# Performance work log

Hardware: AMD Instinct MI355X
Metric: run time of the kernel (lower is better)

## Reference

```python
import jax, jax.numpy as jnp
import numpy as np

N_NODES = 100000
N_EDGES = 600000
F_IN, HID, CLS = 128, 128, 16


def sage_conv(x, src, dst, W_l, b_l, W_r, n_nodes):
    # mean aggregation of neighbor features: message x[src] scattered to dst
    msg = x[src]                                              # [E, F]
    agg = jax.ops.segment_sum(msg, dst, num_segments=n_nodes)  # [N, F]
    deg = jax.ops.segment_sum(jnp.ones((src.shape[0],), x.dtype), dst, num_segments=n_nodes)
    agg = agg / jnp.maximum(deg, 1.0)[:, None]
    # PyG SAGEConv: lin_l(agg) (with bias) + lin_r(x_root) (no bias)
    return agg @ W_l + b_l + x @ W_r


def setup_inputs() -> dict:
    key = jax.random.key(0)
    ks = jax.random.split(key, 6)
    x = jax.random.normal(ks[0], (N_NODES, F_IN), jnp.float32)
    edge_index = jax.random.randint(ks[1], (2, N_EDGES), 0, N_NODES, dtype=jnp.int64)
    s1 = 1.0 / np.sqrt(F_IN)
    s2 = 1.0 / np.sqrt(HID)
    return {
        "x": x,
        "edge_index": edge_index,
        "W1_l": jax.random.normal(ks[2], (F_IN, HID), jnp.float32) * s1,
        "b1": jnp.zeros((HID,), jnp.float32),
        "W1_r": jax.random.normal(ks[3], (F_IN, HID), jnp.float32) * s1,
        "W2_l": jax.random.normal(ks[4], (HID, CLS), jnp.float32) * s2,
        "b2": jnp.zeros((CLS,), jnp.float32),
        "W2_r": jax.random.normal(ks[5], (HID, CLS), jnp.float32) * s2,
    }


def reference(x, edge_index, W1_l, b1, W1_r, W2_l, b2, W2_r):
    n = x.shape[0]
    src, dst = edge_index[0], edge_index[1]
    h = sage_conv(x, src, dst, W1_l, b1, W1_r, n)
    h = jax.nn.relu(h)
    # F.dropout(training=self.training): identity in eval mode
    out = sage_conv(h, src, dst, W2_l, b2, W2_r, n)
    return jax.nn.log_softmax(out, axis=1)
```

## Files before the change

### kernel.cpp

```cpp
#include <hip/hip_runtime.h>
#include <cstdint>

#define N_NODES 100000
#define N_PAD 100096
#define N_EDGES 600000
#define F 128
#define CLS 16
#define CAP 32

typedef short bf16x8 __attribute__((ext_vector_type(8)));
typedef float f32x4 __attribute__((ext_vector_type(4)));

__device__ inline float bf2f(unsigned int lo16) { return __uint_as_float(lo16 << 16); }
__device__ inline unsigned short f2b(float f) {
    unsigned int u = __float_as_uint(f);
    return (unsigned short)((u + 0x7fffu + ((u >> 16) & 1u)) >> 16);
}

__global__ __launch_bounds__(256) void init_k(int* __restrict__ deg,
                                              const float* __restrict__ x,
                                              unsigned short* __restrict__ xb,
                                              const float* __restrict__ W1l,
                                              const float* __restrict__ W1r,
                                              const float* __restrict__ W2l,
                                              const float* __restrict__ W2r,
                                              unsigned short* __restrict__ w1t,
                                              unsigned short* __restrict__ w2t) {
    int b = blockIdx.x;
    if (b < 98) {
        int i = b * 1024 + threadIdx.x * 4;
#pragma unroll
        for (int k = 0; k < 4; k++)
            if (i + k < N_NODES) deg[i + k] = 0;
    } else if (b < 12598) {
        int i = (b - 98) * 256 + threadIdx.x;
        if (i < N_NODES * F / 4) {
            float4 v = ((const float4*)x)[i];
            ushort4 o;
            o.x = f2b(v.x); o.y = f2b(v.y); o.z = f2b(v.z); o.w = f2b(v.w);
            ((ushort4*)xb)[i] = o;
        }
    } else if (b < 12726) {
        int idx = (b - 12598) * 256 + threadIdx.x;
        int n = idx >> 8, k = idx & 255;
        float v = (k < F) ? W1l[k * F + n] : W1r[(k - F) * F + n];
        int ct = n >> 4, m = n & 15;
        int half = k >> 7, ks = (k >> 5) & 3, quad = (k >> 3) & 3, j = k & 7;
        w1t[(ct * 8 + ks * 2 + half) * 512 + (quad * 16 + m) * 8 + j] = f2b(v);
    } else {
        int idx = (b - 12726) * 256 + threadIdx.x;
        if (idx < 32 * F) {
            int n = idx >> 7, k = idx & 127;
            float v = (n < CLS) ? W2l[k * CLS + n] : W2r[k * CLS + (n - CLS)];
            int tile = n >> 4, m = n & 15;
            int ks = (k >> 5) & 3, quad = (k >> 3) & 3, j = k & 7;
            w2t[(tile * 4 + ks) * 512 + (quad * 16 + m) * 8 + j] = f2b(v);
        }
    }
}

__global__ void fill_k(const int* __restrict__ src, const int* __restrict__ dst,
                       int* __restrict__ deg, int* __restrict__ bucket) {
    int e = blockIdx.x * blockDim.x + threadIdx.x;
    if (e < N_EDGES) {
        int d = dst[e];
        int slot = atomicAdd(&deg[d], 1);
        if (slot < CAP) bucket[d * CAP + slot] = src[e];
    }
}

__global__ __launch_bounds__(256) void gemm_fused(const unsigned short* __restrict__ Xb,
                                                  const int* __restrict__ deg,
                                                  const int* __restrict__ bucket,
                                                  const unsigned short* __restrict__ Wt,
                                                  const float* __restrict__ bias,
                                                  const unsigned short* __restrict__ Wt2,
                                                  unsigned short* __restrict__ trLb,
                                                  float* __restrict__ trR) {
    __shared__ unsigned short sh[128 * 136];
    int tid = threadIdx.x;
    int row0 = blockIdx.x * 128;

    int grp = tid >> 4, l16 = tid & 15, f8 = l16 * 8;
#pragma unroll 1
    for (int rr = 0; rr < 8; rr++) {
        int lr = grp * 8 + rr;
        int node = row0 + lr;
        const int* bk = bucket + (size_t)node * CAP;
        int d_raw = deg[node];
        int4 b0 = *(const int4*)(bk);
        int4 b1 = *(const int4*)(bk + 4);
        int4 b2 = *(const int4*)(bk + 8);
        int d = (node < N_NODES) ? min(max(d_raw, 0), CAP) : 0;
        int n0  = (d > 0)  ? min(max(b0.x, 0), N_NODES - 1) : 0;
        int n1  = (d > 1)  ? min(max(b0.y, 0), N_NODES - 1) : 0;
        int n2  = (d > 2)  ? min(max(b0.z, 0), N_NODES - 1) : 0;
        int n3  = (d > 3)  ? min(max(b0.w, 0), N_NODES - 1) : 0;
        int n4  = (d > 4)  ? min(max(b1.x, 0), N_NODES - 1) : 0;
        int n5  = (d > 5)  ? min(max(b1.y, 0), N_NODES - 1) : 0;
        int n6  = (d > 6)  ? min(max(b1.z, 0), N_NODES - 1) : 0;
        int n7  = (d > 7)  ? min(max(b1.w, 0), N_NODES - 1) : 0;
        int n8  = (d > 8)  ? min(max(b2.x, 0), N_NODES - 1) : 0;
        int n9  = (d > 9)  ? min(max(b2.y, 0), N_NODES - 1) : 0;
        int n10 = (d > 10) ? min(max(b2.z, 0), N_NODES - 1) : 0;
        int n11 = (d > 11) ? min(max(b2.w, 0), N_NODES - 1) : 0;
        uint4 v0  = *(const uint4*)(Xb + (size_t)n0 * F + f8);
        uint4 v1  = *(const uint4*)(Xb + (size_t)n1 * F + f8);
        uint4 v2  = *(const uint4*)(Xb + (size_t)n2 * F + f8);
        uint4 v3  = *(const uint4*)(Xb + (size_t)n3 * F + f8);
        uint4 v4  = *(const uint4*)(Xb + (size_t)n4 * F + f8);
        uint4 v5  = *(const uint4*)(Xb + (size_t)n5 * F + f8);
        uint4 v6  = *(const uint4*)(Xb + (size_t)n6 * F + f8);
        uint4 v7  = *(const uint4*)(Xb + (size_t)n7 * F + f8);
        uint4 v8  = *(const uint4*)(Xb + (size_t)n8 * F + f8);
        uint4 v9  = *(const uint4*)(Xb + (size_t)n9 * F + f8);
        uint4 v10 = *(const uint4*)(Xb + (size_t)n10 * F + f8);
        uint4 v11 = *(const uint4*)(Xb + (size_t)n11 * F + f8);

        float acc[8] = {0.f, 0.f, 0.f, 0.f, 0.f, 0.f, 0.f, 0.f};
#define ACC8(vv) { \
        acc[0] += bf2f((vv).x & 0xffffu); acc[1] += bf2f((vv).x >> 16); \
        acc[2] += bf2f((vv).y & 0xffffu); acc[3] += bf2f((vv).y >> 16); \
        acc[4] += bf2f((vv).z & 0xffffu); acc[5] += bf2f((vv).z >> 16); \
        acc[6] += bf2f((vv).w & 0xffffu); acc[7] += bf2f((vv).w >> 16); }
        if (d > 0)  ACC8(v0);
        if (d > 1)  ACC8(v1);
        if (d > 2)  ACC8(v2);
        if (d > 3)  ACC8(v3);
        if (d > 4)  ACC8(v4);
        if (d > 5)  ACC8(v5);
        if (d > 6)  ACC8(v6);
        if (d > 7)  ACC8(v7);
        if (d > 8)  ACC8(v8);
        if (d > 9)  ACC8(v9);
        if (d > 10) ACC8(v10);
        if (d > 11) ACC8(v11);
        for (int j0 = 12; j0 < d; j0 += 4) {
            int4 bb = *(const int4*)(bk + j0);
            int rem = d - j0;
            int m0 = (rem > 0) ? min(max(bb.x, 0), N_NODES - 1) : 0;
            int m1 = (rem > 1) ? min(max(bb.y, 0), N_NODES - 1) : 0;
            int m2 = (rem > 2) ? min(max(bb.z, 0), N_NODES - 1) : 0;
            int m3 = (rem > 3) ? min(max(bb.w, 0), N_NODES - 1) : 0;
            uint4 w0 = *(const uint4*)(Xb + (size_t)m0 * F + f8);
            uint4 w1 = *(const uint4*)(Xb + (size_t)m1 * F + f8);
            uint4 w2 = *(const uint4*)(Xb + (size_t)m2 * F + f8);
            uint4 w3 = *(const uint4*)(Xb + (size_t)m3 * F + f8);
            if (rem > 0) ACC8(w0);
            if (rem > 1) ACC8(w1);
            if (rem > 2) ACC8(w2);
            if (rem > 3) ACC8(w3);
        }
#undef ACC8
        float inv = 1.0f / fmaxf((float)d, 1.0f);
        uint4 o;
        o.x = (unsigned int)f2b(acc[0] * inv) | ((unsigned int)f2b(acc[1] * inv) << 16);
        o.y = (unsigned int)f2b(acc[2] * inv) | ((unsigned int)f2b(acc[3] * inv) << 16);
        o.z = (unsigned int)f2b(acc[4] * inv) | ((unsigned int)f2b(acc[5] * inv) << 16);
        o.w = (unsigned int)f2b(acc[6] * inv) | ((unsigned int)f2b(acc[7] * inv) << 16);
        *(uint4*)&sh[lr * 136 + f8] = o;
    }
    __syncthreads();

    int wave = tid >> 6, lane = tid & 63;
    int m = lane & 15, quad = lane >> 4;
    int koff = quad * 8;
    int wrow0 = row0 + wave * 32;

    const unsigned short* sa0 = sh + (wave * 32 + m) * 136 + koff;
    const unsigned short* sa1 = sa0 + 16 * 136;
    const unsigned short* px0 = Xb + (size_t)(wrow0 + m) * F + koff;
    const unsigned short* px1 = px0 + 16 * F;
    const unsigned short* pw = Wt + lane * 8;

    f32x4 acc0[8], acc1[8];
#pragma unroll
    for (int ct = 0; ct < 8; ct++) { acc0[ct] = (f32x4){0,0,0,0}; acc1[ct] = (f32x4){0,0,0,0}; }

#pragma unroll
    for (int ks = 0; ks < 4; ks++) {
        bf16x8 a0 = *(const bf16x8*)(const void*)(sa0 + ks * 32);
        bf16x8 a1 = *(const bf16x8*)(const void*)(sa1 + ks * 32);
        bf16x8 x0 = *(const bf16x8*)(const void*)(px0 + ks * 32);
        bf16x8 x1 = *(const bf16x8*)(const void*)(px1 + ks * 32);
#pragma unroll
        for (int ct = 0; ct < 8; ct++) {
            bf16x8 bl = *(const bf16x8*)(const void*)(pw + (ct * 8 + ks * 2 + 0) * 512);
            bf16x8 br = *(const bf16x8*)(const void*)(pw + (ct * 8 + ks * 2 + 1) * 512);
            acc0[ct] = __builtin_amdgcn_mfma_f32_16x16x32_bf16(a0, bl, acc0[ct], 0, 0, 0);
            acc1[ct] = __builtin_amdgcn_mfma_f32_16x16x32_bf16(a1, bl, acc1[ct], 0, 0, 0);
            acc0[ct] = __builtin_amdgcn_mfma_f32_16x16x32_bf16(x0, br, acc0[ct], 0, 0, 0);
            acc1[ct] = __builtin_amdgcn_mfma_f32_16x16x32_bf16(x1, br, acc1[ct], 0, 0, 0);
        }
    }
    __syncthreads();

    int lr0 = wave * 32 + quad * 4;
#pragma unroll
    for (int ct = 0; ct < 8; ct++) {
        int n = ct * 16 + m;
        float bv = bias[n];
#pragma unroll
        for (int r = 0; r < 4; r++) {
            sh[(lr0 + r) * 136 + n]      = f2b(fmaxf(acc0[ct][r] + bv, 0.f));
            sh[(lr0 + 16 + r) * 136 + n] = f2b(fmaxf(acc1[ct][r] + bv, 0.f));
        }
    }
    __syncthreads();

    const unsigned short* hl0 = sh + (wave * 32 + m) * 136 + koff;
    const unsigned short* hl1 = hl0 + 16 * 136;
    const unsigned short* pw2 = Wt2 + lane * 8;

    f32x4 al0 = (f32x4){0,0,0,0}, al1 = (f32x4){0,0,0,0};
    f32x4 ar0 = (f32x4){0,0,0,0}, ar1 = (f32x4){0,0,0,0};
#pragma unroll
    for (int ks = 0; ks < 4; ks++) {
        bf16x8 h0 = *(const bf16x8*)(const void*)(hl0 + ks * 32);
        bf16x8 h1 = *(const bf16x8*)(const void*)(hl1 + ks * 32);
        bf16x8 wl = *(const bf16x8*)(const void*)(pw2 + (0 * 4 + ks) * 512);
        bf16x8 wr = *(const bf16x8*)(const void*)(pw2 + (1 * 4 + ks) * 512);
        al0 = __builtin_amdgcn_mfma_f32_16x16x32_bf16(h0, wl, al0, 0, 0, 0);
        al1 = __builtin_amdgcn_mfma_f32_16x16x32_bf16(h1, wl, al1, 0, 0, 0);
        ar0 = __builtin_amdgcn_mfma_f32_16x16x32_bf16(h0, wr, ar0, 0, 0, 0);
        ar1 = __builtin_amdgcn_mfma_f32_16x16x32_bf16(h1, wr, ar1, 0, 0, 0);
    }
    int r0 = wrow0 + quad * 4;
#pragma unroll
    for (int r = 0; r < 4; r++) {
        trLb[(size_t)(r0 + r) * CLS + m]      = f2b(al0[r]);
        trLb[(size_t)(r0 + 16 + r) * CLS + m] = f2b(al1[r]);
        trR[(size_t)(r0 + r) * CLS + m]       = ar0[r];
        trR[(size_t)(r0 + 16 + r) * CLS + m]  = ar1[r];
    }
}

__global__ __launch_bounds__(256) void agg2sm_k(const unsigned short* __restrict__ trLb,
                                                const float* __restrict__ trR,
                                                const int* __restrict__ deg,
                                                const int* __restrict__ bucket,
                                                const float* __restrict__ b2,
                                                float* __restrict__ out) {
    int node = blockIdx.x * 4 + (threadIdx.x >> 6);
    int lane = threadIdx.x & 63;
    int r = lane >> 2;
    int cq = (lane & 3) * 4;
    const int* bk = bucket + node * CAP;

    int d_raw = deg[node];
    int d = min(d_raw, CAP);
    int nb = (r < d) ? min(max(bk[r], 0), N_NODES - 1) : 0;
    uint2 v = *(const uint2*)(trLb + (size_t)nb * CLS + cq);
    float4 selfR = *(const float4*)(trR + (size_t)node * CLS + cq);

    float4 acc = {0.f, 0.f, 0.f, 0.f};
    if (r < d) {
        acc.x += bf2f(v.x & 0xffffu); acc.y += bf2f(v.x >> 16);
        acc.z += bf2f(v.y & 0xffffu); acc.w += bf2f(v.y >> 16);
    }
    if (d > 16) {
        int idx = 16 + r;
        bool valid = idx < d;
        int m2 = valid ? min(max(bk[idx], 0), N_NODES - 1) : 0;
        uint2 w = *(const uint2*)(trLb + (size_t)m2 * CLS + cq);
        if (valid) {
            acc.x += bf2f(w.x & 0xffffu); acc.y += bf2f(w.x >> 16);
            acc.z += bf2f(w.y & 0xffffu); acc.w += bf2f(w.y >> 16);
        }
    }
#pragma unroll
    for (int off = 4; off <= 32; off <<= 1) {
        acc.x += __shfl_xor(acc.x, off);
        acc.y += __shfl_xor(acc.y, off);
        acc.z += __shfl_xor(acc.z, off);
        acc.w += __shfl_xor(acc.w, off);
    }
    float inv = 1.0f / fmaxf((float)d, 1.0f);
    float4 bb = *(const float4*)(b2 + cq);
    float vx = acc.x * inv + selfR.x + bb.x;
    float vy = acc.y * inv + selfR.y + bb.y;
    float vz = acc.z * inv + selfR.z + bb.z;
    float vw = acc.w * inv + selfR.w + bb.w;
    float mx = fmaxf(fmaxf(vx, vy), fmaxf(vz, vw));
    mx = fmaxf(mx, __shfl_xor(mx, 1));
    mx = fmaxf(mx, __shfl_xor(mx, 2));
    float sm = __expf(vx - mx) + __expf(vy - mx) + __expf(vz - mx) + __expf(vw - mx);
    sm += __shfl_xor(sm, 1);
    sm += __shfl_xor(sm, 2);
    float lg = __logf(sm);
    if (r == 0) {
        float4 o = {vx - mx - lg, vy - mx - lg, vz - mx - lg, vw - mx - lg};
        *(float4*)(out + (size_t)node * CLS + cq) = o;
    }
}


extern "C" void kernel_launch(void* const* d_in, const int* in_sizes, int n_in,
                              void* d_out, int out_size, void* d_ws, size_t ws_size,
                              hipStream_t stream) {
    const float* x   = (const float*)d_in[0];
    const int*   ei  = (const int*)d_in[1];
    const float* W1l = (const float*)d_in[2];
    const float* b1  = (const float*)d_in[3];
    const float* W1r = (const float*)d_in[4];
    const float* W2l = (const float*)d_in[5];
    const float* b2  = (const float*)d_in[6];
    const float* W2r = (const float*)d_in[7];
    float* out = (float*)d_out;

    const int* src = ei;
    const int* dst = ei + N_EDGES;

    char* ws = (char*)d_ws;
    size_t off = 0;
    auto alloc = [&](size_t bytes) { char* p = ws + off; off += (bytes + 127) / 128 * 128; return p; };
    int* deg    = (int*)alloc((size_t)N_NODES * 4);
    int* bucket = (int*)alloc((size_t)N_NODES * CAP * 4);
    unsigned short* xb   = (unsigned short*)alloc((size_t)N_PAD * F * 2);
    unsigned short* trLb = (unsigned short*)alloc((size_t)N_PAD * CLS * 2);
    float*          trR  = (float*)alloc((size_t)N_PAD * CLS * 4);
    unsigned short* w1t  = (unsigned short*)alloc((size_t)F * 256 * 2);
    unsigned short* w2t  = (unsigned short*)alloc((size_t)32 * F * 2);

    init_k<<<12743, 256, 0, stream>>>(deg, x, xb, W1l, W1r, W2l, W2r, w1t, w2t);
    fill_k<<<(N_EDGES + 255) / 256, 256, 0, stream>>>(src, dst, deg, bucket);
    gemm_fused<<<N_PAD / 128, 256, 0, stream>>>(xb, deg, bucket, w1t, b1, w2t, trLb, trR);
    agg2sm_k<<<N_NODES / 4, 256, 0, stream>>>(trLb, trR, deg, bucket, b2, out);
}
```

Baseline: 217.0 us.

## Stage neighbor buckets in LDS and double-buffer gathers across node rows

Neighbor index lists and degrees for the block's 128 nodes are loaded cooperatively into shared memory up front. The per-row gather loop is then software-pipelined with two register sets, so the 12 feature gathers for the next row are issued before the current row is accumulated. The aim is to hide gather latency and raise memory-level parallelism in the aggregation phase. The cost is many more live VGPRs (two sets of 12 uint4 values), which may reduce occupancy. It also relies on each row's staged bucket being written and read by the same wave, since there is no barrier between staging and use.

```diff
diff --git a/kernel.cpp b/kernel.cpp
--- a/kernel.cpp
+++ b/kernel.cpp
@@ -81,85 +81,127 @@
     int tid = threadIdx.x;
     int row0 = blockIdx.x * 128;
 
+    {
+        int ns = tid >> 1, half = tid & 1;
+        const int4* gsrc = (const int4*)(bucket + (size_t)(row0 + ns) * CAP + half * 16);
+        int* drow = (int*)(sh + ns * 136);
+        int4* ldst = (int4*)(drow + half * 16);
+        ldst[0] = gsrc[0];
+        ldst[1] = gsrc[1];
+        ldst[2] = gsrc[2];
+        ldst[3] = gsrc[3];
+        if (half == 0) drow[32] = deg[row0 + ns];
+    }
+
     int grp = tid >> 4, l16 = tid & 15, f8 = l16 * 8;
-#pragma unroll 1
-    for (int rr = 0; rr < 8; rr++) {
-        int lr = grp * 8 + rr;
-        int node = row0 + lr;
-        const int* bk = bucket + (size_t)node * CAP;
-        int d_raw = deg[node];
-        int4 b0 = *(const int4*)(bk);
-        int4 b1 = *(const int4*)(bk + 4);
-        int4 b2 = *(const int4*)(bk + 8);
-        int d = (node < N_NODES) ? min(max(d_raw, 0), CAP) : 0;
-        int n0  = (d > 0)  ? min(max(b0.x, 0), N_NODES - 1) : 0;
-        int n1  = (d > 1)  ? min(max(b0.y, 0), N_NODES - 1) : 0;
-        int n2  = (d > 2)  ? min(max(b0.z, 0), N_NODES - 1) : 0;
-        int n3  = (d > 3)  ? min(max(b0.w, 0), N_NODES - 1) : 0;
-        int n4  = (d > 4)  ? min(max(b1.x, 0), N_NODES - 1) : 0;
-        int n5  = (d > 5)  ? min(max(b1.y, 0), N_NODES - 1) : 0;
-        int n6  = (d > 6)  ? min(max(b1.z, 0), N_NODES - 1) : 0;
-        int n7  = (d > 7)  ? min(max(b1.w, 0), N_NODES - 1) : 0;
-        int n8  = (d > 8)  ? min(max(b2.x, 0), N_NODES - 1) : 0;
-        int n9  = (d > 9)  ? min(max(b2.y, 0), N_NODES - 1) : 0;
-        int n10 = (d > 10) ? min(max(b2.z, 0), N_NODES - 1) : 0;
-        int n11 = (d > 11) ? min(max(b2.w, 0), N_NODES - 1) : 0;
-        uint4 v0  = *(const uint4*)(Xb + (size_t)n0 * F + f8);
-        uint4 v1  = *(const uint4*)(Xb + (size_t)n1 * F + f8);
-        uint4 v2  = *(const uint4*)(Xb + (size_t)n2 * F + f8);
-        uint4 v3  = *(const uint4*)(Xb + (size_t)n3 * F + f8);
-        uint4 v4  = *(const uint4*)(Xb + (size_t)n4 * F + f8);
-        uint4 v5  = *(const uint4*)(Xb + (size_t)n5 * F + f8);
-        uint4 v6  = *(const uint4*)(Xb + (size_t)n6 * F + f8);
-        uint4 v7  = *(const uint4*)(Xb + (size_t)n7 * F + f8);
-        uint4 v8  = *(const uint4*)(Xb + (size_t)n8 * F + f8);
-        uint4 v9  = *(const uint4*)(Xb + (size_t)n9 * F + f8);
-        uint4 v10 = *(const uint4*)(Xb + (size_t)n10 * F + f8);
-        uint4 v11 = *(const uint4*)(Xb + (size_t)n11 * F + f8);
-
-        float acc[8] = {0.f, 0.f, 0.f, 0.f, 0.f, 0.f, 0.f, 0.f};
+    int lrb = grp * 8;
+
+#define ISSUE(P, DV, LR) do { \
+    const int* brow_ = (const int*)(sh + (LR) * 136); \
+    int node_ = row0 + (LR); \
+    int draw_ = brow_[32]; \
+    DV = (node_ < N_NODES) ? min(max(draw_, 0), CAP) : 0; \
+    int4 b0_ = ((const int4*)brow_)[0]; \
+    int4 b1_ = ((const int4*)brow_)[1]; \
+    int4 b2_ = ((const int4*)brow_)[2]; \
+    int n0_  = (DV > 0 ) ? min(max(b0_.x, 0), N_NODES - 1) : 0; \
+    int n1_  = (DV > 1 ) ? min(max(b0_.y, 0), N_NODES - 1) : 0; \
+    int n2_  = (DV > 2 ) ? min(max(b0_.z, 0), N_NODES - 1) : 0; \
+    int n3_  = (DV > 3 ) ? min(max(b0_.w, 0), N_NODES - 1) : 0; \
+    int n4_  = (DV > 4 ) ? min(max(b1_.x, 0), N_NODES - 1) : 0; \
+    int n5_  = (DV > 5 ) ? min(max(b1_.y, 0), N_NODES - 1) : 0; \
+    int n6_  = (DV > 6 ) ? min(max(b1_.z, 0), N_NODES - 1) : 0; \
+    int n7_  = (DV > 7 ) ? min(max(b1_.w, 0), N_NODES - 1) : 0; \
+    int n8_  = (DV > 8 ) ? min(max(b2_.x, 0), N_NODES - 1) : 0; \
+    int n9_  = (DV > 9 ) ? min(max(b2_.y, 0), N_NODES - 1) : 0; \
+    int n10_ = (DV > 10) ? min(max(b2_.z, 0), N_NODES - 1) : 0; \
+    int n11_ = (DV > 11) ? min(max(b2_.w, 0), N_NODES - 1) : 0; \
+    P##0  = *(const uint4*)(Xb + (size_t)n0_  * F + f8); \
+    P##1  = *(const uint4*)(Xb + (size_t)n1_  * F + f8); \
+    P##2  = *(const uint4*)(Xb + (size_t)n2_  * F + f8); \
+    P##3  = *(const uint4*)(Xb + (size_t)n3_  * F + f8); \
+    P##4  = *(const uint4*)(Xb + (size_t)n4_  * F + f8); \
+    P##5  = *(const uint4*)(Xb + (size_t)n5_  * F + f8); \
+    P##6  = *(const uint4*)(Xb + (size_t)n6_  * F + f8); \
+    P##7  = *(const uint4*)(Xb + (size_t)n7_  * F + f8); \
+    P##8  = *(const uint4*)(Xb + (size_t)n8_  * F + f8); \
+    P##9  = *(const uint4*)(Xb + (size_t)n9_  * F + f8); \
+    P##10 = *(const uint4*)(Xb + (size_t)n10_ * F + f8); \
+    P##11 = *(const uint4*)(Xb + (size_t)n11_ * F + f8); \
+} while (0)
+
 #define ACC8(vv) { \
-        acc[0] += bf2f((vv).x & 0xffffu); acc[1] += bf2f((vv).x >> 16); \
-        acc[2] += bf2f((vv).y & 0xffffu); acc[3] += bf2f((vv).y >> 16); \
-        acc[4] += bf2f((vv).z & 0xffffu); acc[5] += bf2f((vv).z >> 16); \
-        acc[6] += bf2f((vv).w & 0xffffu); acc[7] += bf2f((vv).w >> 16); }
-        if (d > 0)  ACC8(v0);
-        if (d > 1)  ACC8(v1);
-        if (d > 2)  ACC8(v2);
-        if (d > 3)  ACC8(v3);
-        if (d > 4)  ACC8(v4);
-        if (d > 5)  ACC8(v5);
-        if (d > 6)  ACC8(v6);
-        if (d > 7)  ACC8(v7);
-        if (d > 8)  ACC8(v8);
-        if (d > 9)  ACC8(v9);
-        if (d > 10) ACC8(v10);
-        if (d > 11) ACC8(v11);
-        for (int j0 = 12; j0 < d; j0 += 4) {
-            int4 bb = *(const int4*)(bk + j0);
-            int rem = d - j0;
-            int m0 = (rem > 0) ? min(max(bb.x, 0), N_NODES - 1) : 0;
-            int m1 = (rem > 1) ? min(max(bb.y, 0), N_NODES - 1) : 0;
-            int m2 = (rem > 2) ? min(max(bb.z, 0), N_NODES - 1) : 0;
-            int m3 = (rem > 3) ? min(max(bb.w, 0), N_NODES - 1) : 0;
-            uint4 w0 = *(const uint4*)(Xb + (size_t)m0 * F + f8);
-            uint4 w1 = *(const uint4*)(Xb + (size_t)m1 * F + f8);
-            uint4 w2 = *(const uint4*)(Xb + (size_t)m2 * F + f8);
-            uint4 w3 = *(const uint4*)(Xb + (size_t)m3 * F + f8);
-            if (rem > 0) ACC8(w0);
-            if (rem > 1) ACC8(w1);
-            if (rem > 2) ACC8(w2);
-            if (rem > 3) ACC8(w3);
-        }
+    acc_[0] += bf2f((vv).x & 0xffffu); acc_[1] += bf2f((vv).x >> 16); \
+    acc_[2] += bf2f((vv).y & 0xffffu); acc_[3] += bf2f((vv).y >> 16); \
+    acc_[4] += bf2f((vv).z & 0xffffu); acc_[5] += bf2f((vv).z >> 16); \
+    acc_[6] += bf2f((vv).w & 0xffffu); acc_[7] += bf2f((vv).w >> 16); }
+
+#define CONSUME(P, DV, LR) do { \
+    float acc_[8] = {0.f, 0.f, 0.f, 0.f, 0.f, 0.f, 0.f, 0.f}; \
+    if (DV > 0)  ACC8(P##0); \
+    if (DV > 1)  ACC8(P##1); \
+    if (DV > 2)  ACC8(P##2); \
+    if (DV > 3)  ACC8(P##3); \
+    if (DV > 4)  ACC8(P##4); \
+    if (DV > 5)  ACC8(P##5); \
+    if (DV > 6)  ACC8(P##6); \
+    if (DV > 7)  ACC8(P##7); \
+    if (DV > 8)  ACC8(P##8); \
+    if (DV > 9)  ACC8(P##9); \
+    if (DV > 10) ACC8(P##10); \
+    if (DV > 11) ACC8(P##11); \
+    if (DV > 12) { \
+        const int* brow_ = (const int*)(sh + (LR) * 136); \
+        for (int j0 = 12; j0 < DV; j0 += 4) { \
+            int4 bb_ = *(const int4*)(brow_ + j0); \
+            int rem_ = DV - j0; \
+            int m0_ = (rem_ > 0) ? min(max(bb_.x, 0), N_NODES - 1) : 0; \
+            int m1_ = (rem_ > 1) ? min(max(bb_.y, 0), N_NODES - 1) : 0; \
+            int m2_ = (rem_ > 2) ? min(max(bb_.z, 0), N_NODES - 1) : 0; \
+            int m3_ = (rem_ > 3) ? min(max(bb_.w, 0), N_NODES - 1) : 0; \
+            uint4 w0_ = *(const uint4*)(Xb + (size_t)m0_ * F + f8); \
+            uint4 w1_ = *(const uint4*)(Xb + (size_t)m1_ * F + f8); \
+            uint4 w2_ = *(const uint4*)(Xb + (size_t)m2_ * F + f8); \
+            uint4 w3_ = *(const uint4*)(Xb + (size_t)m3_ * F + f8); \
+            if (rem_ > 0) ACC8(w0_); \
+            if (rem_ > 1) ACC8(w1_); \
+            if (rem_ > 2) ACC8(w2_); \
+            if (rem_ > 3) ACC8(w3_); \
+        } \
+    } \
+    float inv_ = 1.0f / fmaxf((float)DV, 1.0f); \
+    uint4 o_; \
+    o_.x = (unsigned int)f2b(acc_[0] * inv_) | ((unsigned int)f2b(acc_[1] * inv_) << 16); \
+    o_.y = (unsigned int)f2b(acc_[2] * inv_) | ((unsigned int)f2b(acc_[3] * inv_) << 16); \
+    o_.z = (unsigned int)f2b(acc_[4] * inv_) | ((unsigned int)f2b(acc_[5] * inv_) << 16); \
+    o_.w = (unsigned int)f2b(acc_[6] * inv_) | ((unsigned int)f2b(acc_[7] * inv_) << 16); \
+    *(uint4*)&sh[(LR) * 136 + f8] = o_; \
+} while (0)
+
+    {
+        uint4 vA0, vA1, vA2, vA3, vA4, vA5, vA6, vA7, vA8, vA9, vA10, vA11;
+        uint4 vB0, vB1, vB2, vB3, vB4, vB5, vB6, vB7, vB8, vB9, vB10, vB11;
+        int dA, dB;
+        ISSUE(vA, dA, lrb + 0);
+        ISSUE(vB, dB, lrb + 1);
+        CONSUME(vA, dA, lrb + 0);
+        ISSUE(vA, dA, lrb + 2);
+        CONSUME(vB, dB, lrb + 1);
+        ISSUE(vB, dB, lrb + 3);
+        CONSUME(vA, dA, lrb + 2);
+        ISSUE(vA, dA, lrb + 4);
+        CONSUME(vB, dB, lrb + 3);
+        ISSUE(vB, dB, lrb + 5);
+        CONSUME(vA, dA, lrb + 4);
+        ISSUE(vA, dA, lrb + 6);
+        CONSUME(vB, dB, lrb + 5);
+        ISSUE(vB, dB, lrb + 7);
+        CONSUME(vA, dA, lrb + 6);
+        CONSUME(vB, dB, lrb + 7);
+    }
+#undef ISSUE
 #undef ACC8
-        float inv = 1.0f / fmaxf((float)d, 1.0f);
-        uint4 o;
-        o.x = (unsigned int)f2b(acc[0] * inv) | ((unsigned int)f2b(acc[1] * inv) << 16);
-        o.y = (unsigned int)f2b(acc[2] * inv) | ((unsigned int)f2b(acc[3] * inv) << 16);
-        o.z = (unsigned int)f2b(acc[4] * inv) | ((unsigned int)f2b(acc[5] * inv) << 16);
-        o.w = (unsigned int)f2b(acc[6] * inv) | ((unsigned int)f2b(acc[7] * inv) << 16);
-        *(uint4*)&sh[lr * 136 + f8] = o;
-    }
+#undef CONSUME
     __syncthreads();
 
     int wave = tid >> 6, lane = tid & 63;
```

Result: faster. 211.1 us (-2.7%).
